# Performance work log

Hardware: AMD Instinct MI355X
Metric: run time of the kernel (lower is better)

## Reference

```python
import jax, jax.numpy as jnp
import numpy as np

B, S, D = 8, 2048, 512
H, DK, DV = 8, 64, 64


def setup_inputs() -> dict:
    key = jax.random.key(0)
    ks = jax.random.split(key, 12)
    def xavier(k, shape):
        fan_in, fan_out = shape[0], shape[1]
        std = (2.0 / (fan_in + fan_out)) ** 0.5
        return jax.random.normal(k, shape, dtype=jnp.float32) * std
    return {
        "Q": jax.random.normal(ks[0], (B, S, D), dtype=jnp.float32),
        "K": jax.random.normal(ks[1], (B, S, D), dtype=jnp.float32),
        "V": jax.random.normal(ks[2], (B, S, D), dtype=jnp.float32),
        "W_q": xavier(ks[3], (D, H * DK)),
        "W_k": xavier(ks[4], (D, H * DK)),
        "W_v": xavier(ks[5], (D, H * DV)),
        "W_o": xavier(ks[6], (H * DV, D)),
        "W1": xavier(ks[7], (D, D)),  # linear1.weight, stored [out, in]
        "b1": jnp.zeros((D,), dtype=jnp.float32),
        "W2": xavier(ks[8], (D, D)),  # linear2.weight
        "b2": jnp.zeros((D,), dtype=jnp.float32),
    }


def reference(Q, K, V, W_q, W_k, W_v, W_o, W1, b1, W2, b2):
    eps = 1e-6
    bsz, q_len, _ = Q.shape
    # project and split heads: [B, S, H, dk]
    Qh = (Q @ W_q).reshape(bsz, q_len, H, DK)
    Kh = (K @ W_k).reshape(bsz, q_len, H, DK)
    Vh = (V @ W_v).reshape(bsz, q_len, H, DV)
    temperature = DK ** 0.5
    # scores: [B, H, Sq, Sk] (full O(N^2) matrix, as in original)
    scores = jnp.einsum('bqhd,bkhd->bhqk', Qh, Kh) / (temperature + eps)
    probs = jax.nn.softmax(scores, axis=-1)  # dropout = identity (eval)
    V_att = jnp.einsum('bhqk,bkhd->bqhd', probs, Vh).reshape(bsz, q_len, H * DV)
    attn_out = V_att @ W_o  # dropout = identity
    X = Q + attn_out
    # FFN: linear2(relu(linear1(X))); torch Linear: x @ W.T + b
    ffn = jax.nn.relu(X @ W1.T + b1) @ W2.T + b2
    return ffn + X
```

## Files before the change

### kernel.cpp

```cpp
#include <hip/hip_runtime.h>
#include <stdint.h>

typedef __bf16 bf16;
typedef bf16 bf16x8 __attribute__((ext_vector_type(8)));
typedef bf16 bf16x4 __attribute__((ext_vector_type(4)));
typedef float f32x2 __attribute__((ext_vector_type(2)));
typedef float f32x4 __attribute__((ext_vector_type(4)));
typedef float f32x16 __attribute__((ext_vector_type(16)));

#define AS1 __attribute__((address_space(1)))
#define AS3 __attribute__((address_space(3)))

__device__ __forceinline__ void gll16(const void* g, void* l) {
    __builtin_amdgcn_global_load_lds((const AS1 unsigned int*)g,
                                     (AS3 unsigned int*)l, 16, 0, 0);
}

__device__ __forceinline__ bf16 f2bf(float x) { return (bf16)x; }

__device__ __forceinline__ float fexp2(float x) { return __builtin_amdgcn_exp2f(x); }

#define QSCALE_LOG2E 0.18033685757f

__global__ void k_castw(const float* __restrict__ Wq, const float* __restrict__ Wk,
                        const float* __restrict__ Wv, const float* __restrict__ Wo,
                        const float* __restrict__ W1, const float* __restrict__ W2,
                        bf16* __restrict__ oq, bf16* __restrict__ ok, bf16* __restrict__ ov,
                        bf16* __restrict__ oo, bf16* __restrict__ o1, bf16* __restrict__ o2)
{
    const int z = blockIdx.y;
    const int idx = blockIdx.x * 256 + threadIdx.x;
    const float* src = z == 0 ? Wq : z == 1 ? Wk : z == 2 ? Wv : z == 3 ? Wo : z == 4 ? W1 : W2;
    bf16* dst = z == 0 ? oq : z == 1 ? ok : z == 2 ? ov : z == 3 ? oo : z == 4 ? o1 : o2;
    if (z < 4) {
        const int n = idx >> 9, k = idx & 511;
        dst[idx] = f2bf(src[(k << 9) + n]);
    } else {
        dst[idx] = f2bf(src[idx]);
    }
}

__device__ __forceinline__ void gemm_core(const bf16* __restrict__ A,
                                          const bf16* __restrict__ Bt,
                                          const int K, bf16* As, bf16* Bs,
                                          const int bm, const int bn,
                                          f32x4 acc[4][4])
{
    const int tid  = threadIdx.x;
    const int lane = tid & 63;
    const int wave = tid >> 6;
    const int g    = lane >> 4;
    const int l15  = lane & 15;
    const int wm   = (wave >> 1) * 64;
    const int wn   = (wave & 1) * 64;

    const int srow = tid >> 2;
    const int sk   = (tid & 3) * 8;
    const size_t aoff0 = (size_t)(bm + srow) * K + sk;
    const size_t aoff1 = (size_t)(bm + 64 + srow) * K + sk;
    const size_t boff0 = (size_t)(bn + srow) * K + sk;
    const size_t boff1 = (size_t)(bn + 64 + srow) * K + sk;
    char* asb = (char*)As + wave * 1024;
    char* bsb = (char*)Bs + wave * 1024;

    for (int kt = 0; kt < K; kt += 32) {
        __syncthreads();
        gll16(A + aoff0 + kt, asb);
        gll16(A + aoff1 + kt, asb + 4096);
        gll16(Bt + boff0 + kt, bsb);
        gll16(Bt + boff1 + kt, bsb + 4096);
        __syncthreads();
        bf16x8 af[4], bfv[4];
#pragma unroll
        for (int mi = 0; mi < 4; ++mi)
            af[mi] = *(const bf16x8*)&As[(wm + mi * 16 + l15) * 32 + g * 8];
#pragma unroll
        for (int ni = 0; ni < 4; ++ni)
            bfv[ni] = *(const bf16x8*)&Bs[(wn + ni * 16 + l15) * 32 + g * 8];
#pragma unroll
        for (int mi = 0; mi < 4; ++mi)
#pragma unroll
            for (int ni = 0; ni < 4; ++ni)
                acc[mi][ni] = __builtin_amdgcn_mfma_f32_16x16x32_bf16(
                    af[mi], bfv[ni], acc[mi][ni], 0, 0, 0);
    }
}

template<int EPI>
__global__ __launch_bounds__(256)
void k_gemm(const bf16* __restrict__ A, const bf16* __restrict__ Bt,
            const float* __restrict__ bias, const float* __restrict__ residf,
            const bf16* __restrict__ residb,
            float* __restrict__ Cf, bf16* __restrict__ Cb,
            int M, int N, int K)
{
    __shared__ bf16 As[128 * 32];
    __shared__ bf16 Bs[128 * 32];
    const int bm = blockIdx.y * 128, bn = blockIdx.x * 128;
    f32x4 acc[4][4] = {};
    gemm_core(A, Bt, K, As, Bs, bm, bn, acc);

    const int tid  = threadIdx.x;
    const int lane = tid & 63;
    const int wave = tid >> 6;
    const int g    = lane >> 4;
    const int l15  = lane & 15;
    const int wm   = (wave >> 1) * 64;
    const int wn   = (wave & 1) * 64;
    const int col0 = bn + wn + l15;
#pragma unroll
    for (int ni = 0; ni < 4; ++ni) {
        const int col = col0 + ni * 16;
        float bv = 0.f;
        if constexpr (EPI == 2 || EPI == 3) bv = bias[col];
#pragma unroll
        for (int mi = 0; mi < 4; ++mi) {
#pragma unroll
            for (int r = 0; r < 4; ++r) {
                const int row = bm + wm + mi * 16 + 4 * g + r;
                const size_t idx = (size_t)row * N + col;
                float v = acc[mi][ni][r];
                if constexpr (EPI == 1) {
                    Cb[idx] = f2bf(v + residf[idx]);
                } else if constexpr (EPI == 2) {
                    Cb[idx] = f2bf(fmaxf(v + bv, 0.f));
                } else {
                    Cf[idx] = v + bv + (float)residb[idx];
                }
            }
        }
    }
}

__global__ __launch_bounds__(512, 4)
void k_proj(const float* __restrict__ Qf, const float* __restrict__ Kf, const float* __restrict__ Vf,
            const bf16* __restrict__ BQ, const bf16* __restrict__ BK, const bf16* __restrict__ BV,
            bf16* __restrict__ OQ, bf16* __restrict__ OK_, bf16* __restrict__ OV)
{
    __shared__ char SM[65536];
    const int z = blockIdx.y;
    const float* A = z == 0 ? Qf : z == 1 ? Kf : Vf;
    const bf16* Bt = z == 0 ? BQ : z == 1 ? BK : BV;
    bf16* Cb       = z == 0 ? OQ : z == 1 ? OK_ : OV;
    const int tid  = threadIdx.x;
    const int lane = tid & 63;
    const int w    = tid >> 6;
    const int g    = lane >> 4;
    const int l15  = lane & 15;
    const int bm   = blockIdx.x * 64;
    const int bb   = bm >> 11;
    const int s0   = bm & 2047;

    const int arow = tid >> 3, ak0 = (tid & 7) * 4;
    const size_t abase = (size_t)(bm + arow) * 512 + ak0;
    const bf16* bbase = Bt + (size_t)(w * 64 + l15) * 512 + g * 8;

    f32x4 acc[4][4] = {};

    for (int kt = 0; kt < 512; kt += 32) {
        __syncthreads();
        {
            float4 a = *(const float4*)(A + abase + kt);
            bf16x4 c;
            c[0] = f2bf(a.x); c[1] = f2bf(a.y); c[2] = f2bf(a.z); c[3] = f2bf(a.w);
            *(bf16x4*)(SM + tid * 8) = c;
        }
        bf16x8 bfv[4];
#pragma unroll
        for (int ni = 0; ni < 4; ++ni)
            bfv[ni] = *(const bf16x8*)(bbase + (size_t)ni * 16 * 512 + kt);
        __syncthreads();
        bf16x8 af[4];
#pragma unroll
        for (int mi = 0; mi < 4; ++mi)
            af[mi] = *(const bf16x8*)(SM + (mi * 16 + l15) * 64 + g * 16);
#pragma unroll
        for (int mi = 0; mi < 4; ++mi)
#pragma unroll
            for (int ni = 0; ni < 4; ++ni)
                acc[mi][ni] = __builtin_amdgcn_mfma_f32_16x16x32_bf16(
                    af[mi], bfv[ni], acc[mi][ni], 0, 0, 0);
    }

    __syncthreads();
    char* img = SM + w * 8192;
    if (z == 0) {
#pragma unroll
        for (int ni = 0; ni < 4; ++ni) {
            const int dk = ni * 16 + l15;
#pragma unroll
            for (int mi = 0; mi < 4; ++mi)
#pragma unroll
                for (int r = 0; r < 4; ++r) {
                    const int sl = mi * 16 + 4 * g + r;
                    *(bf16*)(img + (sl * 64 + dk) * 2) = f2bf(acc[mi][ni][r] * QSCALE_LOG2E);
                }
        }
    } else if (z == 1) {
#pragma unroll
        for (int ni = 0; ni < 4; ++ni) {
            const int dk = ni * 16 + l15;
            const int ks = dk >> 4, h2 = (dk >> 3) & 1, e = dk & 7;
#pragma unroll
            for (int mi = 0; mi < 4; ++mi)
#pragma unroll
                for (int r = 0; r < 4; ++r) {
                    const int sl = mi * 16 + 4 * g + r;
                    const int t2 = sl >> 5, ql = sl & 31;
                    *(bf16*)(img + (((t2 * 4 + ks) * 64 + h2 * 32 + ql) * 8 + e) * 2) =
                        f2bf(acc[mi][ni][r]);
                }
        }
    } else {
#pragma unroll
        for (int ni = 0; ni < 4; ++ni) {
            const int dk = ni * 16 + l15;
            const int dvt = dk >> 5, ql = dk & 31;
#pragma unroll
            for (int mi = 0; mi < 4; ++mi)
#pragma unroll
                for (int r = 0; r < 4; ++r) {
                    const int sl = mi * 16 + 4 * g + r;
                    const int ktile = sl >> 4, kk = sl & 15;
                    const int h2 = (kk >> 2) & 1;
                    const int e = (kk & 3) | ((kk >> 3) << 2);
                    *(bf16*)(img + (((dvt * 4 + ktile) * 64 + h2 * 32 + ql) * 8 + e) * 2) =
                        f2bf(acc[mi][ni][r]);
                }
        }
    }
    __syncthreads();
#pragma unroll
    for (int i = 0; i < 8; ++i) {
        const int G = i * 512 + tid;
        const int hl = G >> 9;
        const size_t a0 = (size_t)(bb * 8 + hl) * 131072;
        const size_t slab = (z == 0) ? a0 + (size_t)s0 * 64
                                     : a0 + (size_t)(s0 >> 6) * 4096;
        bf16x8 v = *(const bf16x8*)(SM + G * 16);
        *(bf16x8*)&Cb[slab + (size_t)(G & 511) * 8] = v;
    }
}

__global__ __launch_bounds__(256, 2)
void k_attn(const bf16* __restrict__ Qp, const bf16* __restrict__ Khp,
            const bf16* __restrict__ Vtp, bf16* __restrict__ O)
{
    __shared__ bf16 smem[16384];
    const int tid = threadIdx.x;
    const int l   = tid & 63;
    const int w   = tid >> 6;
    const int h   = l >> 5;
    const int ql  = l & 31;
    const int d   = blockIdx.x;
    const int bh  = ((d >> 6) << 3) | (d & 7);
    const int qt  = (d >> 3) & 7;
    const size_t base = (size_t)bh * 131072;
    const int q0 = qt * 256 + w * 64;
    const int loff = l * 16;

    bf16x8 qfA[4], qfB[4];
#pragma unroll
    for (int ks = 0; ks < 4; ++ks) {
        qfA[ks] = *(const bf16x8*)&Qp[base + (size_t)(q0 + ql) * 64 + ks * 16 + h * 8];
        qfB[ks] = *(const bf16x8*)&Qp[base + (size_t)(q0 + 32 + ql) * 64 + ks * 16 + h * 8];
    }

    f32x16 oA0 = {}, oA1 = {}, oB0 = {}, oB1 = {};
    float lrunA = 0.f, lrunB = 0.f;

    const bf16* ksrc = Khp + base + tid * 8;
    const bf16* vsrc = Vtp + base + tid * 8;
    char* kb0 = (char*)smem;
    char* kb1 = (char*)smem + 16384;
    const int wdst = w * 1024;

    auto stage = [&](int kvt, char* kb) {
        const bf16* ks = ksrc + kvt * 4096;
        const bf16* vs = vsrc + kvt * 4096;
        gll16(ks,        kb + wdst);
        gll16(ks + 2048, kb + 4096 + wdst);
        gll16(vs,        kb + 8192 + wdst);
        gll16(vs + 2048, kb + 12288 + wdst);
    };

    auto compute = [&](const char* kb) {
        f32x16 sA0 = {}, sA1 = {}, sB0 = {}, sB1 = {};
        __builtin_amdgcn_s_setprio(1);
#pragma unroll
        for (int ks = 0; ks < 4; ++ks) {
            bf16x8 a0 = *(const bf16x8*)(kb + ks * 1024 + loff);
            bf16x8 a1 = *(const bf16x8*)(kb + 4096 + ks * 1024 + loff);
            sA0 = __builtin_amdgcn_mfma_f32_32x32x16_bf16(a0, qfA[ks], sA0, 0, 0, 0);
            sB0 = __builtin_amdgcn_mfma_f32_32x32x16_bf16(a0, qfB[ks], sB0, 0, 0, 0);
            sA1 = __builtin_amdgcn_mfma_f32_32x32x16_bf16(a1, qfA[ks], sA1, 0, 0, 0);
            sB1 = __builtin_amdgcn_mfma_f32_32x32x16_bf16(a1, qfB[ks], sB1, 0, 0, 0);
        }
        __builtin_amdgcn_s_setprio(0);

        f32x2 pA = {0.f, 0.f}, pB = {0.f, 0.f};
#pragma unroll
        for (int r = 0; r < 16; r += 2) {
            sA0[r]     = fexp2(sA0[r]);
            sA0[r + 1] = fexp2(sA0[r + 1]);
            sA1[r]     = fexp2(sA1[r]);
            sA1[r + 1] = fexp2(sA1[r + 1]);
            pA += (f32x2){sA0[r], sA0[r + 1]};
            pA += (f32x2){sA1[r], sA1[r + 1]};
        }
#pragma unroll
        for (int r = 0; r < 16; r += 2) {
            sB0[r]     = fexp2(sB0[r]);
            sB0[r + 1] = fexp2(sB0[r + 1]);
            sB1[r]     = fexp2(sB1[r]);
            sB1[r + 1] = fexp2(sB1[r + 1]);
            pB += (f32x2){sB0[r], sB0[r + 1]};
            pB += (f32x2){sB1[r], sB1[r + 1]};
        }
        lrunA += pA[0] + pA[1];
        lrunB += pB[0] + pB[1];

        bf16x8 pbA[4], pbB[4];
#pragma unroll
        for (int j = 0; j < 4; ++j) {
            const int ofs = 8 * (j & 1);
#pragma unroll
            for (int e = 0; e < 8; ++e) {
                pbA[j][e] = f2bf((j & 2) ? sA1[ofs + e] : sA0[ofs + e]);
                pbB[j][e] = f2bf((j & 2) ? sB1[ofs + e] : sB0[ofs + e]);
            }
        }

        const char* vr = kb + 8192;
        __builtin_amdgcn_s_setprio(1);
#pragma unroll
        for (int j = 0; j < 4; ++j) {
            bf16x8 a0 = *(const bf16x8*)(vr + j * 1024 + loff);
            bf16x8 a1 = *(const bf16x8*)(vr + 4096 + j * 1024 + loff);
            oA0 = __builtin_amdgcn_mfma_f32_32x32x16_bf16(a0, pbA[j], oA0, 0, 0, 0);
            oB0 = __builtin_amdgcn_mfma_f32_32x32x16_bf16(a0, pbB[j], oB0, 0, 0, 0);
            oA1 = __builtin_amdgcn_mfma_f32_32x32x16_bf16(a1, pbA[j], oA1, 0, 0, 0);
            oB1 = __builtin_amdgcn_mfma_f32_32x32x16_bf16(a1, pbB[j], oB1, 0, 0, 0);
        }
        __builtin_amdgcn_s_setprio(0);
    };

    stage(0, kb0);
    __syncthreads();
    for (int kvt = 0; kvt < 32; kvt += 2) {
        if (kvt + 1 < 32) stage(kvt + 1, kb1);
        compute(kb0);
        __syncthreads();
        if (kvt + 2 < 32) stage(kvt + 2, kb0);
        compute(kb1);
        __syncthreads();
    }

    char* ot = (char*)smem + w * 4096;
    const int qr = l >> 1;
    const int dh4 = (l & 1) * 4;
    auto epi = [&](const f32x16& e0, const f32x16& e1, float lr, int qg) {
        lr += __shfl_xor(lr, 32);
        const float inv = 1.f / lr;
#pragma unroll
        for (int dvt = 0; dvt < 2; ++dvt) {
#pragma unroll
            for (int r = 0; r < 16; ++r) {
                const int dv = dvt * 32 + (r & 3) + 8 * (r >> 2) + 4 * h;
                const float val = (dvt ? e1[r] : e0[r]) * inv;
                *(bf16*)(ot + ql * 128 + ((((dv >> 3) ^ (ql & 7)) << 4) | ((dv & 7) << 1))) = f2bf(val);
            }
        }
        const size_t ob = ((size_t)(bh >> 3) * 2048 + qg + qr) * 512 + (bh & 7) * 64 + (size_t)dh4 * 8;
#pragma unroll
        for (int B = 0; B < 4; ++B) {
            bf16x8 v = *(const bf16x8*)(ot + qr * 128 + (((dh4 + B) ^ (qr & 7)) << 4));
            *(bf16x8*)&O[ob + B * 8] = v;
        }
    };
    epi(oA0, oA1, lrunA, q0);
    epi(oB0, oB1, lrunB, q0 + 32);
}

extern "C" void kernel_launch(void* const* d_in, const int* in_sizes, int n_in,
                              void* d_out, int out_size, void* d_ws, size_t ws_size,
                              hipStream_t stream)
{
    const float* Q  = (const float*)d_in[0];
    const float* K  = (const float*)d_in[1];
    const float* V  = (const float*)d_in[2];
    const float* Wq = (const float*)d_in[3];
    const float* Wk = (const float*)d_in[4];
    const float* Wv = (const float*)d_in[5];
    const float* Wo = (const float*)d_in[6];
    const float* W1 = (const float*)d_in[7];
    const float* b1 = (const float*)d_in[8];
    const float* W2 = (const float*)d_in[9];
    const float* b2 = (const float*)d_in[10];
    float* out = (float*)d_out;

    const int M = 8 * 2048;
    const size_t TN = (size_t)M * 512;
    const int WN = 512 * 512;

    char* ws = (char*)d_ws;
    bf16* Qhp  = (bf16*)ws;
    bf16* Khp  = Qhp + TN;
    bf16* Vtp  = Khp + TN;
    bf16* Vatt = Vtp + TN;
    bf16* H1   = Vatt + TN;
    bf16* Xbf  = H1 + TN;
    bf16* Wqt  = Xbf + TN;
    bf16* Wkt  = Wqt + WN;
    bf16* Wvt  = Wkt + WN;
    bf16* Wot  = Wvt + WN;
    bf16* W1b  = Wot + WN;
    bf16* W2b  = W1b + WN;

    k_castw<<<dim3(1024, 6), 256, 0, stream>>>(Wq, Wk, Wv, Wo, W1, W2,
                                               Wqt, Wkt, Wvt, Wot, W1b, W2b);

    k_proj<<<dim3(256, 3), 512, 0, stream>>>(Q, K, V, Wqt, Wkt, Wvt,
                                             Qhp, Khp, Vtp);

    k_attn<<<512, 256, 0, stream>>>(Qhp, Khp, Vtp, Vatt);

    dim3 gg(4, 128);
    k_gemm<1><<<gg, 256, 0, stream>>>(Vatt, Wot, nullptr, Q, nullptr, nullptr, Xbf, M, 512, 512);
    k_gemm<2><<<gg, 256, 0, stream>>>(Xbf, W1b, b1, nullptr, nullptr, nullptr, H1, M, 512, 512);
    k_gemm<3><<<gg, 256, 0, stream>>>(H1, W2b, b2, nullptr, Xbf, out, nullptr, M, 512, 512);
}
```

Measured before the change: 206.4 us.

## Double-buffer projection GEMM with LDS-staged swizzled weights via global_load_lds

Restructures the QKV projection kernel's K-loop into a two-stage double-buffered pipeline. The next tile's weights are loaded asynchronously into LDS with global_load_lds while the current tile is computed. The A tile is also stored with an XOR swizzle. Weight fragments now come from swizzled LDS instead of direct per-lane global loads, and there is one barrier per stage instead of two. The goal is to hide global memory latency and cut LDS bank conflicts. In exchange, LDS use grows to 72KB, which may reduce occupancy below the declared launch bounds.

After: 192.3 us. 6.8% less time.

```diff
diff --git a/kernel.cpp b/kernel.cpp
--- a/kernel.cpp
+++ b/kernel.cpp
@@ -137,7 +137,7 @@
             const bf16* __restrict__ BQ, const bf16* __restrict__ BK, const bf16* __restrict__ BV,
             bf16* __restrict__ OQ, bf16* __restrict__ OK_, bf16* __restrict__ OV)
 {
-    __shared__ char SM[65536];
+    __shared__ char SM[73728];
     const int z = blockIdx.y;
     const float* A = z == 0 ? Qf : z == 1 ? Kf : Vf;
     const bf16* Bt = z == 0 ? BQ : z == 1 ? BK : BV;
@@ -151,38 +151,66 @@
     const int bb   = bm >> 11;
     const int s0   = bm & 2047;
 
-    const int arow = tid >> 3, ak0 = (tid & 7) * 4;
-    const size_t abase = (size_t)(bm + arow) * 512 + ak0;
-    const bf16* bbase = Bt + (size_t)(w * 64 + l15) * 512 + g * 8;
+    const int arow = tid >> 3;
+    const size_t aoff = (size_t)(bm + arow) * 512 + (tid & 7) * 4;
+    const int awr = arow * 64 + ((((tid >> 1) & 3) ^ ((arow >> 1) & 3)) << 4) + (tid & 1) * 8;
+    const int brow = tid >> 2;
+    const size_t boff = (size_t)brow * 512 + (((tid & 3) ^ ((tid >> 3) & 3)) << 3);
+    int ard[4], brd[4];
+#pragma unroll
+    for (int mi = 0; mi < 4; ++mi) {
+        const int r2 = mi * 16 + l15;
+        ard[mi] = r2 * 64 + ((g ^ ((r2 >> 1) & 3)) << 4);
+    }
+#pragma unroll
+    for (int ni = 0; ni < 4; ++ni) {
+        const int col = w * 64 + ni * 16 + l15;
+        brd[ni] = 4096 + col * 64 + ((g ^ ((col >> 1) & 3)) << 4);
+    }
 
     f32x4 acc[4][4] = {};
 
-    for (int kt = 0; kt < 512; kt += 32) {
-        __syncthreads();
-        {
-            float4 a = *(const float4*)(A + abase + kt);
-            bf16x4 c;
-            c[0] = f2bf(a.x); c[1] = f2bf(a.y); c[2] = f2bf(a.z); c[3] = f2bf(a.w);
-            *(bf16x4*)(SM + tid * 8) = c;
-        }
-        bf16x8 bfv[4];
+    auto stage = [&](int s, int bufsel) {
+        char* buf = SM + bufsel * 36864;
+        const bf16* bsrc = Bt + boff + s * 32;
+        char* bdst = buf + 4096 + w * 1024;
+#pragma unroll
+        for (int i = 0; i < 4; ++i)
+            gll16(bsrc + (size_t)i * 65536, bdst + i * 8192);
+        float4 a = *(const float4*)(A + aoff + s * 32);
+        bf16x4 c;
+        c[0] = f2bf(a.x); c[1] = f2bf(a.y); c[2] = f2bf(a.z); c[3] = f2bf(a.w);
+        *(bf16x4*)(buf + awr) = c;
+    };
+
+    auto compute = [&](int bufsel) {
+        const char* buf = SM + bufsel * 36864;
+        bf16x8 af[4], bfv[4];
+#pragma unroll
+        for (int mi = 0; mi < 4; ++mi)
+            af[mi] = *(const bf16x8*)(buf + ard[mi]);
 #pragma unroll
         for (int ni = 0; ni < 4; ++ni)
-            bfv[ni] = *(const bf16x8*)(bbase + (size_t)ni * 16 * 512 + kt);
-        __syncthreads();
-        bf16x8 af[4];
-#pragma unroll
-        for (int mi = 0; mi < 4; ++mi)
-            af[mi] = *(const bf16x8*)(SM + (mi * 16 + l15) * 64 + g * 16);
+            bfv[ni] = *(const bf16x8*)(buf + brd[ni]);
 #pragma unroll
         for (int mi = 0; mi < 4; ++mi)
 #pragma unroll
             for (int ni = 0; ni < 4; ++ni)
                 acc[mi][ni] = __builtin_amdgcn_mfma_f32_16x16x32_bf16(
                     af[mi], bfv[ni], acc[mi][ni], 0, 0, 0);
-    }
-
+    };
+
+    stage(0, 0);
     __syncthreads();
+    for (int s = 0; s < 16; s += 2) {
+        if (s + 1 < 16) stage(s + 1, 1);
+        compute(0);
+        __syncthreads();
+        if (s + 2 < 16) stage(s + 2, 0);
+        compute(1);
+        __syncthreads();
+    }
+
     char* img = SM + w * 8192;
     if (z == 0) {
 #pragma unroll
```
